# Kernel tuning notes

Measured on AMD Instinct MI355X. Metric: run time of the kernel, lower is better.

The kernel has to match this reference:

```python
import jax, jax.numpy as jnp
import numpy as np
import math

B, T, D = 2, 2048, 1024
H = 16
DH = D // H
DFF = 4096
EPS = 1e-5


def setup_inputs() -> dict:
    key = jax.random.key(0)
    ks = jax.random.split(key, 10)
    x = jax.random.normal(ks[0], (B, T, D), dtype=jnp.float32)
    # bool mask, True above diagonal => masked (matches masked_fill semantics)
    causal_mask = jnp.triu(jnp.ones((T, T), dtype=bool), k=1)
    s = 0.02
    return {
        "x": x,
        "causal_mask": causal_mask,
        "gamma1": jnp.ones((D,), jnp.float32),
        "beta1": jnp.zeros((D,), jnp.float32),
        "wq": jax.random.normal(ks[1], (D, D), jnp.float32) * s,
        "wk": jax.random.normal(ks[2], (D, D), jnp.float32) * s,
        "wv": jax.random.normal(ks[3], (D, D), jnp.float32) * s,
        "wo": jax.random.normal(ks[4], (D, D), jnp.float32) * s,
        "gamma2": jnp.ones((D,), jnp.float32),
        "beta2": jnp.zeros((D,), jnp.float32),
        "w1": jax.random.normal(ks[5], (D, DFF), jnp.float32) * s,
        "b1": jnp.zeros((DFF,), jnp.float32),
        "w2": jax.random.normal(ks[6], (DFF, D), jnp.float32) * s,
        "b2": jnp.zeros((D,), jnp.float32),
    }


def _layer_norm(x, gamma, beta):
    mean = jnp.mean(x, axis=-1, keepdims=True)
    var = jnp.mean((x - mean) ** 2, axis=-1, keepdims=True)
    xhat = (x - mean) / jnp.sqrt(var + EPS)
    return gamma * xhat + beta


def _split_heads(x):
    b, t, d = x.shape
    return x.reshape(b, t, H, DH).transpose(0, 2, 1, 3)  # (B,H,T,Dh)


def reference(x, causal_mask, gamma1, beta1, wq, wk, wv, wo,
              gamma2, beta2, w1, b1, w2, b2):
    # --- attention sublayer (pre-LN) ---
    h = _layer_norm(x, gamma1, beta1)
    q = _split_heads(h @ wq)
    k = _split_heads(h @ wk)
    v = _split_heads(h @ wv)
    scores = jnp.einsum('bhqd,bhkd->bhqk', q, k) / math.sqrt(DH)  # (B,H,T,T)
    scores = jnp.where(causal_mask[None, None, :, :], -jnp.inf, scores)
    attn = jax.nn.softmax(scores, axis=-1)
    out = jnp.einsum('bhqk,bhkd->bhqd', attn, v)
    out = out.transpose(0, 2, 1, 3).reshape(x.shape)  # merge heads
    attn_out = out @ wo
    x = x + attn_out
    # --- FFN sublayer (pre-LN) ---
    h = _layer_norm(x, gamma2, beta2)
    ffn = jax.nn.gelu(h @ w1 + b1, approximate=False) @ w2 + b2
    return x + ffn
```

## Files before the change

kernel.cpp:

```cpp
#include <hip/hip_runtime.h>
#include <hip/hip_bf16.h>
#include <math.h>

#define B_   2
#define T_   2048
#define D_   1024
#define H_   16
#define DH_  64
#define DFF_ 4096
#define NTOK (B_*T_)

typedef __attribute__((ext_vector_type(8))) short short8;
typedef __attribute__((ext_vector_type(4))) float f32x4;

static __device__ __forceinline__ short f2bf(float f) {
    union { __hip_bfloat16 h; short s; } u;
    u.h = __float2bfloat16(f);
    return u.s;
}

static __device__ __forceinline__ f32x4 mfma16(short8 a, short8 b, f32x4 c) {
    return __builtin_amdgcn_mfma_f32_16x16x32_bf16(a, b, c, 0, 0, 0);
}

static __device__ __forceinline__ void gload16(const void* g, void* l) {
    __builtin_amdgcn_global_load_lds(
        (__attribute__((address_space(1))) void*)g,
        (__attribute__((address_space(3))) void*)l, 16, 0, 0);
}

static __device__ __forceinline__ short8 lds_read_sw(const short* base, int row, int kbyte) {
    const int off = (row << 7) + (kbyte ^ ((row & 7) << 4));
    return *reinterpret_cast<const short8*>(reinterpret_cast<const char*>(base) + off);
}

__global__ __launch_bounds__(256) void transpose_cast(
    const float* __restrict__ src, short* __restrict__ dst, int K, int N, float scale)
{
    __shared__ short tile[32][33];
    const int k0 = blockIdx.y * 32, n0 = blockIdx.x * 32;
    const int tx = threadIdx.x, ty = threadIdx.y;
    #pragma unroll
    for (int j = 0; j < 4; ++j) {
        int k = ty + j * 8;
        tile[k][tx] = f2bf(src[(size_t)(k0 + k) * N + n0 + tx] * scale);
    }
    __syncthreads();
    #pragma unroll
    for (int j = 0; j < 4; ++j) {
        int n = ty + j * 8;
        dst[(size_t)(n0 + n) * K + k0 + tx] = tile[tx][n];
    }
}

__global__ __launch_bounds__(256) void ln_kernel(
    const float* __restrict__ in, const float* __restrict__ gamma,
    const float* __restrict__ beta, short* __restrict__ out)
{
    const int row = blockIdx.x;
    const int t = threadIdx.x;
    const float4 v = *reinterpret_cast<const float4*>(in + (size_t)row * D_ + t * 4);
    float s  = v.x + v.y + v.z + v.w;
    float sq = v.x*v.x + v.y*v.y + v.z*v.z + v.w*v.w;
    #pragma unroll
    for (int off = 32; off >= 1; off >>= 1) {
        s  += __shfl_xor(s, off);
        sq += __shfl_xor(sq, off);
    }
    __shared__ float ps[4], pq[4];
    if ((t & 63) == 0) { ps[t >> 6] = s; pq[t >> 6] = sq; }
    __syncthreads();
    s  = ps[0] + ps[1] + ps[2] + ps[3];
    sq = pq[0] + pq[1] + pq[2] + pq[3];
    const float mean = s * (1.0f / D_);
    float var = sq * (1.0f / D_) - mean * mean;
    var = fmaxf(var, 0.0f);
    const float rstd = rsqrtf(var + 1e-5f);
    const float4 g = *reinterpret_cast<const float4*>(gamma + t * 4);
    const float4 b = *reinterpret_cast<const float4*>(beta  + t * 4);
    short4 o;
    o.x = f2bf(g.x * ((v.x - mean) * rstd) + b.x);
    o.y = f2bf(g.y * ((v.y - mean) * rstd) + b.y);
    o.z = f2bf(g.z * ((v.z - mean) * rstd) + b.z);
    o.w = f2bf(g.w * ((v.w - mean) * rstd) + b.w);
    *reinterpret_cast<short4*>(out + (size_t)row * D_ + t * 4) = o;
}

template<int BM, int BN, int WR, int WC, int EPI>
__global__ __launch_bounds__(256) void gemm_kernel(
    const short* __restrict__ A, const short* __restrict__ Bt,
    void* __restrict__ Cout, const float* __restrict__ resid,
    const float* __restrict__ bias, int M, int N, int K, int nbx)
{
    constexpr int MB = BM / WR / 16;
    constexpr int NB = BN / WC / 16;
    __shared__ short As[BM * 64];
    __shared__ short Bs[BN * 64];
    const int t = threadIdx.x;
    const int wid = t >> 6, lane = t & 63;
    const int lr = lane & 15, lk = lane >> 4;
    const int cpx = (int)gridDim.x >> 3;
    const int bid = (int)blockIdx.x;
    const int swz = (bid & 7) * cpx + (bid >> 3);
    const int m0 = (swz / nbx) * BM, n0 = (swz % nbx) * BN;
    const int wrow = (wid / WC) * (BM / WR);
    const int wcol = (wid % WC) * (BN / WC);

    f32x4 acc[MB][NB];
    #pragma unroll
    for (int m = 0; m < MB; ++m)
        #pragma unroll
        for (int n = 0; n < NB; ++n) acc[m][n] = (f32x4){0.f, 0.f, 0.f, 0.f};

    for (int k0 = 0; k0 < K; k0 += 64) {
        #pragma unroll
        for (int j = 0; j < BM / 32; ++j) {
            const int off = j * 4096 + t * 16;
            const int r   = off >> 7;
            const int cb  = (off & 127) ^ ((r & 7) << 4);
            gload16(A + (size_t)(m0 + r) * K + k0 + (cb >> 1),
                    (char*)As + j * 4096 + wid * 1024);
        }
        #pragma unroll
        for (int j = 0; j < BN / 32; ++j) {
            const int off = j * 4096 + t * 16;
            const int r   = off >> 7;
            const int cb  = (off & 127) ^ ((r & 7) << 4);
            gload16(Bt + (size_t)(n0 + r) * K + k0 + (cb >> 1),
                    (char*)Bs + j * 4096 + wid * 1024);
        }
        __syncthreads();
        #pragma unroll
        for (int kk = 0; kk < 64; kk += 32) {
            short8 af[MB], bf[NB];
            #pragma unroll
            for (int m = 0; m < MB; ++m)
                af[m] = lds_read_sw(As, wrow + m * 16 + lr, (kk + lk * 8) * 2);
            #pragma unroll
            for (int n = 0; n < NB; ++n)
                bf[n] = lds_read_sw(Bs, wcol + n * 16 + lr, (kk + lk * 8) * 2);
            #pragma unroll
            for (int m = 0; m < MB; ++m)
                #pragma unroll
                for (int n = 0; n < NB; ++n)
                    acc[m][n] = mfma16(af[m], bf[n], acc[m][n]);
        }
        __syncthreads();
    }

    #pragma unroll
    for (int m = 0; m < MB; ++m) {
        #pragma unroll
        for (int n = 0; n < NB; ++n) {
            #pragma unroll
            for (int r = 0; r < 4; ++r) {
                const int gr = m0 + wrow + m * 16 + lk * 4 + r;
                const int gc = n0 + wcol + n * 16 + lr;
                const size_t idx = (size_t)gr * N + gc;
                const float v = acc[m][n][r];
                if constexpr (EPI == 0) {
                    ((short*)Cout)[idx] = f2bf(v);
                } else if constexpr (EPI == 1) {
                    ((float*)Cout)[idx] = resid[idx] + v;
                } else if constexpr (EPI == 2) {
                    const float tt = v + bias[gc];
                    const float ge = 0.5f * tt * (1.0f + erff(tt * 0.70710678118654752f));
                    ((short*)Cout)[idx] = f2bf(ge);
                } else {
                    ((float*)Cout)[idx] = resid[idx] + v + bias[gc];
                }
            }
        }
    }
}

__global__ __launch_bounds__(512) void vtrans(
    const short* __restrict__ qkv, short* __restrict__ vT)
{
    __shared__ short tile[64][65];
    const int qt = blockIdx.x;
    const int bh = blockIdx.y;
    const int b = bh >> 4, h = bh & 15;
    const int tx = threadIdx.x, ty = threadIdx.y;
    const short* src = qkv + ((size_t)(b * T_ + qt * 64)) * 3072 + 2048 + h * 64;
    #pragma unroll
    for (int j = 0; j < 8; ++j) {
        int tl = ty + j * 8;
        tile[tl][tx] = src[(size_t)tl * 3072 + tx];
    }
    __syncthreads();
    short* dst = vT + ((size_t)bh * 64) * T_ + qt * 64;
    #pragma unroll
    for (int j = 0; j < 8; ++j) {
        int dh = ty + j * 8;
        dst[(size_t)dh * T_ + tx] = tile[tx][dh];
    }
}

__global__ __launch_bounds__(256) void attn_kernel(
    const short* __restrict__ qkv, const short* __restrict__ vT,
    short* __restrict__ attn)
{
    __shared__ short Ks[2][4096];
    __shared__ short Vs[2][4096];
    __shared__ short Ps[4][1024];
    const int xx = blockIdx.x;
    const int bh = blockIdx.y;
    const int a  = xx & 7, bq = xx >> 3;
    const int i2 = ((bh >> 3) + bq) & 3;
    const int qt = (i2 == 0) ? a : (i2 == 1) ? 31 - a : (i2 == 2) ? 8 + a : 23 - a;
    const int b = bh >> 4, h = bh & 15;
    const int t = threadIdx.x;
    const int wid = t >> 6, lane = t & 63;
    const int lr = lane & 15, lk = lane >> 4;
    const int q0 = qt * 64 + wid * 16;

    const short* qrow = qkv + (size_t)(b * T_ + q0 + lr) * 3072 + h * 64;
    const short8 qf0 = *reinterpret_cast<const short8*>(qrow + lk * 8);
    const short8 qf1 = *reinterpret_cast<const short8*>(qrow + 32 + lk * 8);
    const short* kbase = qkv + (size_t)b * T_ * 3072 + 1024 + h * 64;
    const short* vbase = vT + (size_t)bh * 64 * T_;

    f32x4 o[4];
    float mr[4], lsp[4];
    #pragma unroll
    for (int n = 0; n < 4; ++n) o[n] = (f32x4){0.f, 0.f, 0.f, 0.f};
    #pragma unroll
    for (int r = 0; r < 4; ++r) { mr[r] = -INFINITY; lsp[r] = 0.f; }

    const int nkt = qt + 1;

    #pragma unroll
    for (int j = 0; j < 2; ++j) {
        const int off = j * 4096 + t * 16;
        const int r   = off >> 7;
        const int cb  = (off & 127) ^ ((r & 7) << 4);
        gload16(kbase + (size_t)r * 3072 + (cb >> 1), (char*)Ks[0] + j * 4096 + wid * 1024);
        gload16(vbase + (size_t)r * T_   + (cb >> 1), (char*)Vs[0] + j * 4096 + wid * 1024);
    }
    __syncthreads();

    int cur = 0;
    for (int kt = 0; kt < nkt; ++kt) {
        const int kvb = kt * 64;
        if (kt + 1 < nkt) {
            const int nb = kvb + 64;
            #pragma unroll
            for (int j = 0; j < 2; ++j) {
                const int off = j * 4096 + t * 16;
                const int r   = off >> 7;
                const int cb  = (off & 127) ^ ((r & 7) << 4);
                gload16(kbase + (size_t)(nb + r) * 3072 + (cb >> 1),
                        (char*)Ks[cur ^ 1] + j * 4096 + wid * 1024);
                gload16(vbase + (size_t)r * T_ + nb + (cb >> 1),
                        (char*)Vs[cur ^ 1] + j * 4096 + wid * 1024);
            }
        }

        f32x4 s[4];
        #pragma unroll
        for (int n = 0; n < 4; ++n) s[n] = (f32x4){0.f, 0.f, 0.f, 0.f};
        #pragma unroll
        for (int n = 0; n < 4; ++n) {
            s[n] = mfma16(qf0, lds_read_sw(Ks[cur], n * 16 + lr, (lk * 8) * 2), s[n]);
            s[n] = mfma16(qf1, lds_read_sw(Ks[cur], n * 16 + lr, (32 + lk * 8) * 2), s[n]);
        }

        const bool needmask = (kt == qt);
        char* pw = (char*)&Ps[wid][0];
        #pragma unroll
        for (int r = 0; r < 4; ++r) {
            const int qg = q0 + lk * 4 + r;
            float v0 = s[0][r], v1 = s[1][r], v2 = s[2][r], v3 = s[3][r];
            if (needmask) {
                if (kvb +      lr > qg) v0 = -INFINITY;
                if (kvb + 16 + lr > qg) v1 = -INFINITY;
                if (kvb + 32 + lr > qg) v2 = -INFINITY;
                if (kvb + 48 + lr > qg) v3 = -INFINITY;
            }
            const float mxl = fmaxf(fmaxf(v0, v1), fmaxf(v2, v3));
            if (!__all(mxl <= mr[r] + 8.0f)) {
                float mx = mxl;
                mx = fmaxf(mx, __shfl_xor(mx, 1));
                mx = fmaxf(mx, __shfl_xor(mx, 2));
                mx = fmaxf(mx, __shfl_xor(mx, 4));
                mx = fmaxf(mx, __shfl_xor(mx, 8));
                const float mnew = fmaxf(mr[r], mx);
                const float alpha = __builtin_amdgcn_exp2f(mr[r] - mnew);
                o[0][r] *= alpha; o[1][r] *= alpha; o[2][r] *= alpha; o[3][r] *= alpha;
                lsp[r] *= alpha;
                mr[r] = mnew;
            }
            const float p0 = __builtin_amdgcn_exp2f(v0 - mr[r]);
            const float p1 = __builtin_amdgcn_exp2f(v1 - mr[r]);
            const float p2 = __builtin_amdgcn_exp2f(v2 - mr[r]);
            const float p3 = __builtin_amdgcn_exp2f(v3 - mr[r]);
            lsp[r] += p0 + p1 + p2 + p3;
            const int prow = lk * 4 + r;
            const int sw = (prow & 7) << 4;
            char* prb = pw + prow * 128;
            *(short*)(prb + (((     lr * 2)) ^ sw)) = f2bf(p0);
            *(short*)(prb + ((32 + lr * 2) ^ sw)) = f2bf(p1);
            *(short*)(prb + ((64 + lr * 2) ^ sw)) = f2bf(p2);
            *(short*)(prb + ((96 + lr * 2) ^ sw)) = f2bf(p3);
        }
        asm volatile("s_waitcnt lgkmcnt(0)" ::: "memory");

        #pragma unroll
        for (int kk = 0; kk < 2; ++kk) {
            const short8 pf = *reinterpret_cast<const short8*>(
                pw + lr * 128 + ((kk * 64 + lk * 16) ^ ((lr & 7) << 4)));
            #pragma unroll
            for (int n = 0; n < 4; ++n)
                o[n] = mfma16(pf, lds_read_sw(Vs[cur], n * 16 + lr, (kk * 32 + lk * 8) * 2), o[n]);
        }
        __syncthreads();
        cur ^= 1;
    }

    #pragma unroll
    for (int r = 0; r < 4; ++r) {
        float l = lsp[r];
        l += __shfl_xor(l, 1);
        l += __shfl_xor(l, 2);
        l += __shfl_xor(l, 4);
        l += __shfl_xor(l, 8);
        const float inv = 1.0f / l;
        short* op = attn + (size_t)(b * T_ + q0 + lk * 4 + r) * D_ + h * 64;
        #pragma unroll
        for (int n = 0; n < 4; ++n)
            op[n * 16 + lr] = f2bf(o[n][r] * inv);
    }
}

extern "C" void kernel_launch(void* const* d_in, const int* in_sizes, int n_in,
                              void* d_out, int out_size, void* d_ws, size_t ws_size,
                              hipStream_t stream)
{
    (void)in_sizes; (void)n_in; (void)out_size; (void)ws_size;
    const float* x      = (const float*)d_in[0];
    const float* gamma1 = (const float*)d_in[2];
    const float* beta1  = (const float*)d_in[3];
    const float* wq     = (const float*)d_in[4];
    const float* wk     = (const float*)d_in[5];
    const float* wv     = (const float*)d_in[6];
    const float* wo     = (const float*)d_in[7];
    const float* gamma2 = (const float*)d_in[8];
    const float* beta2  = (const float*)d_in[9];
    const float* w1     = (const float*)d_in[10];
    const float* b1     = (const float*)d_in[11];
    const float* w2     = (const float*)d_in[12];
    const float* b2     = (const float*)d_in[13];
    float* out = (float*)d_out;

    char* ws = (char*)d_ws;
    size_t off = 0;
    short* wqkvT = (short*)(ws + off); off += (size_t)3072 * 1024 * 2;
    short* woT   = (short*)(ws + off); off += (size_t)1024 * 1024 * 2;
    short* w1T   = (short*)(ws + off); off += (size_t)4096 * 1024 * 2;
    short* w2T   = (short*)(ws + off); off += (size_t)1024 * 4096 * 2;
    short* h1    = (short*)(ws + off); off += (size_t)NTOK * 1024 * 2;
    short* h2    = (short*)(ws + off); off += (size_t)NTOK * 1024 * 2;
    float* y     = (float*)(ws + off); off += (size_t)NTOK * 1024 * 4;
    short* attnb = (short*)(ws + off); off += (size_t)NTOK * 1024 * 2;
    short* qkv   = (short*)(ws + off); off += (size_t)NTOK * 3072 * 2;
    short* vT    = (short*)(ws + off); off += (size_t)B_ * H_ * DH_ * T_ * 2;
    short* g     = qkv;

    const dim3 tb(32, 8);
    transpose_cast<<<dim3(32, 32),  tb, 0, stream>>>(wq, wqkvT,               1024, 1024, 0.18033688011112042f);
    transpose_cast<<<dim3(32, 32),  tb, 0, stream>>>(wk, wqkvT + 1024 * 1024, 1024, 1024, 1.0f);
    transpose_cast<<<dim3(32, 32),  tb, 0, stream>>>(wv, wqkvT + 2048 * 1024, 1024, 1024, 1.0f);
    transpose_cast<<<dim3(32, 32),  tb, 0, stream>>>(wo, woT,                 1024, 1024, 1.0f);
    transpose_cast<<<dim3(128, 32), tb, 0, stream>>>(w1, w1T, 1024, 4096, 1.0f);
    transpose_cast<<<dim3(32, 128), tb, 0, stream>>>(w2, w2T, 4096, 1024, 1.0f);

    ln_kernel<<<NTOK, 256, 0, stream>>>(x, gamma1, beta1, h1);

    gemm_kernel<128, 128, 2, 2, 0><<<768, 256, 0, stream>>>(
        h1, wqkvT, qkv, nullptr, nullptr, NTOK, 3072, 1024, 24);

    vtrans<<<dim3(T_ / 64, B_ * H_), dim3(64, 8), 0, stream>>>(qkv, vT);

    attn_kernel<<<dim3(T_ / 64, B_ * H_), 256, 0, stream>>>(qkv, vT, attnb);

    gemm_kernel<128, 64, 2, 2, 1><<<512, 256, 0, stream>>>(
        attnb, woT, y, x, nullptr, NTOK, 1024, 1024, 16);

    ln_kernel<<<NTOK, 256, 0, stream>>>(y, gamma2, beta2, h2);

    gemm_kernel<128, 128, 2, 2, 2><<<1024, 256, 0, stream>>>(
        h2, w1T, g, nullptr, b1, NTOK, 4096, 1024, 32);

    gemm_kernel<128, 64, 2, 2, 3><<<512, 256, 0, stream>>>(
        g, w2T, out, y, b2, NTOK, 1024, 4096, 16);
}
```

Baseline: 278.5 us.

## Double-buffer LDS tiles in GEMM to overlap global loads with MFMA

```diff
diff --git a/kernel.cpp b/kernel.cpp
--- a/kernel.cpp
+++ b/kernel.cpp
@@ -94,8 +94,10 @@
 {
     constexpr int MB = BM / WR / 16;
     constexpr int NB = BN / WC / 16;
-    __shared__ short As[BM * 64];
-    __shared__ short Bs[BN * 64];
+    constexpr int JA = BM / 32;
+    constexpr int JB = BN / 32;
+    __shared__ short As[2][BM * 64];
+    __shared__ short Bs[2][BN * 64];
     const int t = threadIdx.x;
     const int wid = t >> 6, lane = t & 63;
     const int lr = lane & 15, lk = lane >> 4;
@@ -106,39 +108,59 @@
     const int wrow = (wid / WC) * (BM / WR);
     const int wcol = (wid % WC) * (BN / WC);
 
+    const char* aSrc[JA];
+    const char* bSrc[JB];
+    #pragma unroll
+    for (int j = 0; j < JA; ++j) {
+        const int off = j * 4096 + t * 16;
+        const int r   = off >> 7;
+        const int cb  = (off & 127) ^ ((r & 7) << 4);
+        aSrc[j] = (const char*)(A + (size_t)(m0 + r) * K) + cb;
+    }
+    #pragma unroll
+    for (int j = 0; j < JB; ++j) {
+        const int off = j * 4096 + t * 16;
+        const int r   = off >> 7;
+        const int cb  = (off & 127) ^ ((r & 7) << 4);
+        bSrc[j] = (const char*)(Bt + (size_t)(n0 + r) * K) + cb;
+    }
+
     f32x4 acc[MB][NB];
     #pragma unroll
     for (int m = 0; m < MB; ++m)
         #pragma unroll
         for (int n = 0; n < NB; ++n) acc[m][n] = (f32x4){0.f, 0.f, 0.f, 0.f};
 
-    for (int k0 = 0; k0 < K; k0 += 64) {
-        #pragma unroll
-        for (int j = 0; j < BM / 32; ++j) {
-            const int off = j * 4096 + t * 16;
-            const int r   = off >> 7;
-            const int cb  = (off & 127) ^ ((r & 7) << 4);
-            gload16(A + (size_t)(m0 + r) * K + k0 + (cb >> 1),
-                    (char*)As + j * 4096 + wid * 1024);
-        }
-        #pragma unroll
-        for (int j = 0; j < BN / 32; ++j) {
-            const int off = j * 4096 + t * 16;
-            const int r   = off >> 7;
-            const int cb  = (off & 127) ^ ((r & 7) << 4);
-            gload16(Bt + (size_t)(n0 + r) * K + k0 + (cb >> 1),
-                    (char*)Bs + j * 4096 + wid * 1024);
-        }
-        __syncthreads();
+    const int NT = K >> 6;
+
+    #pragma unroll
+    for (int j = 0; j < JA; ++j)
+        gload16(aSrc[j], (char*)As[0] + j * 4096 + wid * 1024);
+    #pragma unroll
+    for (int j = 0; j < JB; ++j)
+        gload16(bSrc[j], (char*)Bs[0] + j * 4096 + wid * 1024);
+    __syncthreads();
+
+    int cur = 0;
+    for (int kt = 0; kt < NT; ++kt) {
+        if (kt + 1 < NT) {
+            const int kb = (kt + 1) << 7;
+            #pragma unroll
+            for (int j = 0; j < JA; ++j)
+                gload16(aSrc[j] + kb, (char*)As[cur ^ 1] + j * 4096 + wid * 1024);
+            #pragma unroll
+            for (int j = 0; j < JB; ++j)
+                gload16(bSrc[j] + kb, (char*)Bs[cur ^ 1] + j * 4096 + wid * 1024);
+        }
         #pragma unroll
         for (int kk = 0; kk < 64; kk += 32) {
             short8 af[MB], bf[NB];
             #pragma unroll
             for (int m = 0; m < MB; ++m)
-                af[m] = lds_read_sw(As, wrow + m * 16 + lr, (kk + lk * 8) * 2);
+                af[m] = lds_read_sw(As[cur], wrow + m * 16 + lr, (kk + lk * 8) * 2);
             #pragma unroll
             for (int n = 0; n < NB; ++n)
-                bf[n] = lds_read_sw(Bs, wcol + n * 16 + lr, (kk + lk * 8) * 2);
+                bf[n] = lds_read_sw(Bs[cur], wcol + n * 16 + lr, (kk + lk * 8) * 2);
             #pragma unroll
             for (int m = 0; m < MB; ++m)
                 #pragma unroll
@@ -146,6 +168,7 @@
                     acc[m][n] = mfma16(af[m], bf[n], acc[m][n]);
         }
         __syncthreads();
+        cur ^= 1;
     }
 
     #pragma unroll
```

New measurement: 271.7 us. 2.4% less time.
